# Kernel optimization log

Measured on AMD Instinct MI355X. Metric: run time of the kernel, lower is better.

Reference implementation:

```python
import jax, jax.numpy as jnp
import numpy as np

B, H, NI, NO, T = 128, 256, 2, 10, 64
LAMBDA, ETA, SAMPLE, DECISION = 0.95, 0.5, 32, 8


def _xavier(key, shape):
    fan_in, fan_out = shape
    s = (2.0 / (fan_in + fan_out)) ** 0.5
    return jax.random.normal(key, shape, dtype=jnp.float32) * s


def setup_inputs():
    key = jax.random.key(0)
    ks = jax.random.split(key, 10)
    return {
        "x_in": jax.random.normal(ks[0], (T, B, 5), dtype=jnp.float32),
        "W_sr": _xavier(ks[1], (NI, H)),
        "W_ma": _xavier(ks[2], (NI + 1, H)),
        "W_ro": _xavier(ks[3], (H, H)),
        "W_ao": _xavier(ks[4], (H, H)),
        "W_ar": _xavier(ks[5], (H, H)),
        "W_ra": _xavier(ks[6], (H, H)),
        "W_a": _xavier(ks[7], (H, H)),
        "W_y": _xavier(ks[8], (H, NO)),
        "g": jnp.ones((1, H), dtype=jnp.float32),
        "b": jnp.zeros((1, H), dtype=jnp.float32),
        "time": T,
    }


def _forward(x_in, W_sr, W_ma, W_ro, W_ao, W_ar, W_ra, W_a, W_y, g, b):
    Tn = x_in.shape[0]

    def step(carry, inp):
        r, a, A = carry
        x, t = inp  # x: [B,5]
        a_prev = a
        # ATN / RSC recurrent populations
        a = jax.nn.relu(x[:, NI:] @ W_ma + a @ W_a + r @ W_ra)      # [B,H]
        r = jax.nn.relu(x[:, :NI] @ W_sr + a_prev @ W_ar)           # [B,H]
        # readout through fast-weight memory A: o = ro(r) + r @ A + ao(a)
        o = r @ W_ro + jnp.einsum('bh,bhk->bk', r, A) + a @ W_ao    # [B,H]
        mu = jnp.mean(o, axis=0, keepdims=True)                     # mean over batch
        o = jax.nn.relu(g * (o - mu) + b)
        # Hebbian fast-weight update: A = lambda*A + eta * outer(o, r)
        eta_t = jnp.where(t > SAMPLE, 0.0, ETA)
        A = LAMBDA * A + eta_t * o[:, :, None] * r[:, None, :]      # [B,H,H]
        y = o @ W_y                                                 # [B,NO]
        return (r, a, A), y

    carry0 = (
        jnp.zeros((B, H), jnp.float32),
        jnp.zeros((B, H), jnp.float32),
        jnp.zeros((B, H, H), jnp.float32),
    )
    _, ys = jax.lax.scan(step, carry0, (x_in, jnp.arange(Tn)))
    return ys[-DECISION:]  # [decision, B, n_output]


def reference(x_in, W_sr, W_ma, W_ro, W_ao, W_ar, W_ra, W_a, W_y, g, b, time):
    return _forward(x_in, W_sr, W_ma, W_ro, W_ao, W_ar, W_ra, W_a, W_y, g, b)
```

## Files before the change

### kernel.cpp

```cpp
#include <hip/hip_runtime.h>
#include <hip/hip_fp16.h>


typedef unsigned long long u64;

#define HH 256
#define NSTEPS 64

#define OFF_ST 0u
#define OFF_C  262144u
#define OFF_MU 329728u
#define OFF_H  395264u
#define WS_FLOATS 460800u

#define SENT_STATE   0xBF800000BF800000ull
#define SENT_C       0xBF800000u
#define SENT_MU      0x7FC00000u
#define SENT_MU_PAIR 0x7FC000007FC00000ull

#define AGENT __HIP_MEMORY_SCOPE_AGENT
#define RLX   __ATOMIC_RELAXED

__device__ __forceinline__ u64 ld64(const u64* p){ return __hip_atomic_load(p,RLX,AGENT); }
__device__ __forceinline__ void st64s(u64* p,u64 v){ __hip_atomic_store(p,v,RLX,AGENT); }
__device__ __forceinline__ float ld32f(const float* p){ return __hip_atomic_load(p,RLX,AGENT); }
__device__ __forceinline__ void st32f(float* p,float v){ __hip_atomic_store(p,v,RLX,AGENT); }
__device__ __forceinline__ u64 pack2(float lo,float hi){
  return (u64)__float_as_uint(lo) | ((u64)__float_as_uint(hi)<<32);
}

__global__ __launch_bounds__(256) void smn_init(float* __restrict__ ws,
                                                float* __restrict__ out,
                                                const float* __restrict__ W_ro,
                                                const float* __restrict__ W_ao){
  unsigned i = blockIdx.x*256u + threadIdx.x, st = gridDim.x*256u;
  u64* stp=(u64*)(ws+OFF_ST); float* cp=ws+OFF_C; u64* mp=(u64*)(ws+OFF_MU);
  for (unsigned k=i;k<131072u;k+=st) st64s(&stp[k],SENT_STATE);
  for (unsigned k=i;k<67584u;k+=st)  st32f(&cp[k],__uint_as_float(SENT_C));
  for (unsigned k=i;k<32768u;k+=st)  st64s(&mp[k],SENT_MU_PAIR);
  for (unsigned k=i;k<10240u;k+=st)  out[k]=0.f;
  __half* hro = (__half*)(ws + OFF_H);
  __half* hao = hro + 65536;
  for (unsigned idx=i; idx<65536u; idx+=st) {
    unsigned k = idx >> 8, c = idx & 255u;
    unsigned dst = (c>>6)*16384u + k*64u + (c&63u);
    hro[dst] = __float2half(W_ro[idx]);
    hao[dst] = __float2half(W_ao[idx]);
  }
}

__global__ __launch_bounds__(512) void smn_main(
    const float* __restrict__ x_in, const float* __restrict__ W_sr,
    const float* __restrict__ W_ma, const float* __restrict__ W_ro,
    const float* __restrict__ W_ao, const float* __restrict__ W_ar,
    const float* __restrict__ W_ra, const float* __restrict__ W_a,
    const float* __restrict__ W_y,  const float* __restrict__ gvec,
    const float* __restrict__ bvec, float* __restrict__ out,
    float* __restrict__ ws)
{
  __shared__ __align__(16) float aF[2][HH], rF[2][HH];
  __shared__ __align__(16) float P[2][32][2][64];
  __shared__ __align__(16) float r_hist[33][2][64];
  __shared__ __align__(16) float o_hist[33][2][64];
  __shared__ __align__(8)  __half Wro_l[256][68];
  __shared__ __align__(8)  __half Wao_l[256][68];
  __shared__ float opre[2][64];
  __shared__ float c_l[33][2];
  __shared__ float mu_l[64];
  __shared__ float muG[16][32][2];
  __shared__ float lam_pow[64];
  __shared__ float x_l[2][5];

  const int tid = threadIdx.x;
  const int bid = blockIdx.x;
  const int grp = bid >> 2, jsl = bid & 3;
  const int b0 = grp * 2, c0 = jsl * 64;
  const int q = tid & 15, ks = tid >> 4;

  u64*   st64    = (u64*)(ws + OFF_ST);
  float* c_parts = ws + OFF_C;
  u64*   mu64    = (u64*)(ws + OFF_MU);

  const int cc2 = c0 + (tid & 63);
  const float gv  = gvec[cc2], bv = bvec[cc2];
  const float wma0=W_ma[cc2], wma1=W_ma[HH+cc2], wma2=W_ma[2*HH+cc2];
  const float wsr0=W_sr[cc2], wsr1=W_sr[HH+cc2];
  if (tid < 64) lam_pow[tid] = powf(0.95f,(float)tid);
  if (tid < 10) x_l[tid/5][tid%5] = x_in[(b0 + tid/5)*5 + tid%5];
  {
    const __half* hro = (const __half*)(ws + OFF_H) + jsl*16384;
    const __half* hao = (const __half*)(ws + OFF_H) + 65536 + jsl*16384;
    for (int i = tid; i < 4096; i += 512) {
      int k = i >> 4, c4 = (i & 15) * 4;
      *(uint2*)&Wro_l[k][c4] = *(const uint2*)&hro[k*64 + c4];
      *(uint2*)&Wao_l[k][c4] = *(const uint2*)&hao[k*64 + c4];
    }
  }
  __syncthreads();

  for (int t = 0; t <= NSTEPS; ++t) {
    if (t < NSTEPS) {
      if (t == 0) {
        if (tid < 128) {
          int b = tid>>6, c = tid&63;
          float va = fmaxf(x_l[b][2]*wma0 + x_l[b][3]*wma1 + x_l[b][4]*wma2, 0.f);
          float vr = fmaxf(x_l[b][0]*wsr0 + x_l[b][1]*wsr1, 0.f);
          aF[b][c0+c]=va; rF[b][c0+c]=vr; r_hist[0][b][c]=vr;
          st64s(&st64[(unsigned)((b0+b)*HH + cc2)], pack2(va,vr));
        }
        __syncthreads();
      } else {
        const int kb = ks*8;
        float sa0[8],sa1[8],sr0[8],sr1[8];
        *(float4*)&sa0[0]=*(const float4*)&aF[0][kb]; *(float4*)&sa0[4]=*(const float4*)&aF[0][kb+4];
        *(float4*)&sa1[0]=*(const float4*)&aF[1][kb]; *(float4*)&sa1[4]=*(const float4*)&aF[1][kb+4];
        *(float4*)&sr0[0]=*(const float4*)&rF[0][kb]; *(float4*)&sr0[4]=*(const float4*)&rF[0][kb+4];
        *(float4*)&sr1[0]=*(const float4*)&rF[1][kb]; *(float4*)&sr1[4]=*(const float4*)&rF[1][kb+4];
        float aA[2][4]={{0.f,0.f,0.f,0.f},{0.f,0.f,0.f,0.f}};
        float aR[2][4]={{0.f,0.f,0.f,0.f},{0.f,0.f,0.f,0.f}};
        #pragma unroll
        for (int kk=0; kk<8; ++kk) {
          const int k = kb + kk;
          const float4 wa = *(const float4*)&W_a [k*HH + c0 + q*4];
          const float4 wr = *(const float4*)&W_ra[k*HH + c0 + q*4];
          const float4 wn = *(const float4*)&W_ar[k*HH + c0 + q*4];
          #pragma unroll
          for (int jj=0;jj<4;++jj){
            const float waj=(&wa.x)[jj], wrj=(&wr.x)[jj], wnj=(&wn.x)[jj];
            aA[0][jj] += sa0[kk]*waj + sr0[kk]*wrj;
            aA[1][jj] += sa1[kk]*waj + sr1[kk]*wrj;
            aR[0][jj] += sa0[kk]*wnj;
            aR[1][jj] += sa1[kk]*wnj;
          }
        }
        *(float4*)&P[0][ks][0][q*4] = make_float4(aA[0][0],aA[0][1],aA[0][2],aA[0][3]);
        *(float4*)&P[0][ks][1][q*4] = make_float4(aA[1][0],aA[1][1],aA[1][2],aA[1][3]);
        *(float4*)&P[1][ks][0][q*4] = make_float4(aR[0][0],aR[0][1],aR[0][2],aR[0][3]);
        *(float4*)&P[1][ks][1][q*4] = make_float4(aR[1][0],aR[1][1],aR[1][2],aR[1][3]);
        __syncthreads();
        if (tid < 128) {
          int b=tid>>6, c=tid&63;
          float sa=0.f, sr=0.f;
          #pragma unroll
          for (int e=0;e<32;++e){ sa+=P[0][e][b][c]; sr+=P[1][e][b][c]; }
          float va = fmaxf(sa + x_l[b][2]*wma0 + x_l[b][3]*wma1 + x_l[b][4]*wma2, 0.f);
          float vr = fmaxf(sr + x_l[b][0]*wsr0 + x_l[b][1]*wsr1, 0.f);
          if (t<=32) r_hist[t][b][c]=vr;
          st64s(&st64[(unsigned)((t&3)*32768) + (unsigned)((b0+b)*HH + cc2)], pack2(va,vr));
          aF[b][c0+c]=va; rF[b][c0+c]=vr;
        }
        __syncthreads();
      }
      if (t+1 < NSTEPS && tid < 10)
        x_l[tid/5][tid%5] = x_in[((t+1)*128 + b0 + tid/5)*5 + tid%5];
    }

    const int tp = t - 1;
    const bool fin = (t >= 1) && (tp <= 32 || tp >= 56);
    if (fin) {
      const int m = (tp <= 32) ? tp : tp - 23;
      {
        const int p = tid & 31, ch = tid >> 5;
        const u64* base = &mu64[(unsigned)(((m&3)*4 + jsl)*64)*32u];
        u64 vals[4]; unsigned rm = 0;
        const u64* ptrs[4];
        #pragma unroll
        for (int gg=0; gg<4; ++gg) ptrs[gg] = &base[(unsigned)((ch*4+gg)*32 + p)];
        while (rm != 0xFu) {
          #pragma unroll
          for (int gg=0; gg<4; ++gg) if (!(rm & (1u<<gg))) {
            u64 v = ld64(ptrs[gg]);
            if ((unsigned)v != SENT_MU && (unsigned)(v>>32) != SENT_MU) { vals[gg]=v; rm |= 1u<<gg; }
          }
        }
        float s0=0.f, s1=0.f;
        #pragma unroll
        for (int gg=0; gg<4; ++gg) { s0 += __uint_as_float((unsigned)vals[gg]);
                                     s1 += __uint_as_float((unsigned)(vals[gg]>>32)); }
        muG[ch][p][0]=s0; muG[ch][p][1]=s1;
      }
      __syncthreads();
      if (tid < 32) {
        float s0=0.f,s1=0.f;
        #pragma unroll
        for (int ch2=0;ch2<16;++ch2){ s0+=muG[ch2][tid][0]; s1+=muG[ch2][tid][1]; }
        mu_l[2*tid]=s0*(1.f/128.f); mu_l[2*tid+1]=s1*(1.f/128.f);
        st64s(&mu64[(unsigned)((((m+3)&3)*4 + jsl)*64 + grp)*32u + (unsigned)tid], SENT_MU_PAIR);
      }
      __syncthreads();
      if (tid < 128) {
        int b=tid>>6, c=tid&63;
        float o = fmaxf(gv*(opre[b][c]-mu_l[c]) + bv, 0.f);
        opre[b][c]=o;
        if (tp<=32) o_hist[tp][b][c]=o;
      }
      __syncthreads();
      if (tp >= 56 && tid < 320) {
        int ow=tid>>4, l16=tid&15, b=ow/10, n=ow%10;
        float acc=0.f;
        #pragma unroll
        for (int i2=0;i2<4;++i2){ int c=l16*4+i2; acc += opre[b][c]*W_y[(c0+c)*10+n]; }
        acc+=__shfl_xor(acc,1); acc+=__shfl_xor(acc,2);
        acc+=__shfl_xor(acc,4); acc+=__shfl_xor(acc,8);
        if (l16==0) atomicAdd(&out[(tp-56)*1280 + (b0+b)*10 + n], acc);
      }
    }
    if (t == NSTEPS) break;

    const bool live = (t <= 32 || t >= 56);
    const int mc = (t <= 32) ? t : t - 23;
    const int smax = (t-1 < 32) ? (t-1) : 32;

    if (tid < 128) {
      if (live && smax >= 0) {
        const int l8 = tid & 7;
        for (int pp = tid>>3; pp < (smax+1)*2; pp += 16) {
          const int s = pp>>1, b2 = pp&1;
          float acc=0.f;
          #pragma unroll
          for (int i2=0;i2<8;++i2){ int c=l8*8+i2; acc += rF[b2][c0+c]*o_hist[s][b2][c]; }
          acc+=__shfl_xor(acc,1); acc+=__shfl_xor(acc,2); acc+=__shfl_xor(acc,4);
          if (l8==0) st32f(&c_parts[(unsigned)((((mc&3)*33+s)*128 + b0+b2)*4 + jsl)], acc);
        }
      }
    } else {
      const int w = tid - 128;
      const int pi = w >> 7, w2 = w & 127, b = w2>>6, c64 = w2&63;
      const int jp = (jsl + 1 + pi) & 3;
      const u64* ptr = &st64[(unsigned)((t&3)*32768) + (unsigned)((b0+b)*HH + jp*64 + c64)];
      u64 v;
      for (;;){ v = ld64(ptr); if (v != SENT_STATE) break; }
      aF[b][jp*64+c64] = __uint_as_float((unsigned)v);
      rF[b][jp*64+c64] = __uint_as_float((unsigned)(v>>32));
    }
    __syncthreads();
    if (tid < 128) {
      int b=tid>>6;
      st64s(&st64[(unsigned)(((t+3)&3)*32768) + (unsigned)((b0+b)*HH + cc2)], SENT_STATE);
    }

    if (live) {
      const int kb = ks*8;
      float sa0[8],sa1[8],sr0[8],sr1[8];
      *(float4*)&sa0[0]=*(const float4*)&aF[0][kb]; *(float4*)&sa0[4]=*(const float4*)&aF[0][kb+4];
      *(float4*)&sa1[0]=*(const float4*)&aF[1][kb]; *(float4*)&sa1[4]=*(const float4*)&aF[1][kb+4];
      *(float4*)&sr0[0]=*(const float4*)&rF[0][kb]; *(float4*)&sr0[4]=*(const float4*)&rF[0][kb+4];
      *(float4*)&sr1[0]=*(const float4*)&rF[1][kb]; *(float4*)&sr1[4]=*(const float4*)&rF[1][kb+4];
      float aO[2][4]={{0.f,0.f,0.f,0.f},{0.f,0.f,0.f,0.f}};
      #pragma unroll
      for (int kk=0;kk<8;++kk){
        const int k=kb+kk;
        const __half2* ro2 = (const __half2*)&Wro_l[k][q*4];
        const __half2* ao2 = (const __half2*)&Wao_l[k][q*4];
        const float2 wo01 = __half22float2(ro2[0]), wo23 = __half22float2(ro2[1]);
        const float2 wq01 = __half22float2(ao2[0]), wq23 = __half22float2(ao2[1]);
        const float wof[4] = {wo01.x, wo01.y, wo23.x, wo23.y};
        const float wqf[4] = {wq01.x, wq01.y, wq23.x, wq23.y};
        #pragma unroll
        for (int jj=0;jj<4;++jj){
          aO[0][jj] += sr0[kk]*wof[jj] + sa0[kk]*wqf[jj];
          aO[1][jj] += sr1[kk]*wof[jj] + sa1[kk]*wqf[jj];
        }
      }
      *(float4*)&P[0][ks][0][q*4] = make_float4(aO[0][0],aO[0][1],aO[0][2],aO[0][3]);
      *(float4*)&P[0][ks][1][q*4] = make_float4(aO[1][0],aO[1][1],aO[1][2],aO[1][3]);
      if (smax >= 0 && tid < (smax+1)*8) {
        const int s=tid>>3, b2=(tid>>2)&1, jj2=tid&3;
        const float* ptr=&c_parts[(unsigned)((((mc&3)*33+s)*128 + b0+b2)*4 + jj2)];
        float v;
        for(;;){ v=ld32f(ptr); if (__float_as_uint(v)!=SENT_C) break; }
        v+=__shfl_xor(v,1); v+=__shfl_xor(v,2);
        if (jj2==0) c_l[s][b2]=v;
      }
      __syncthreads();
      if (smax >= 0 && tid >= 128 && tid < 194) {
        const int s=(tid-128)>>1, b2=(tid-128)&1;
        st32f(&c_parts[(unsigned)(((((mc+3)&3)*33+s)*128 + b0+b2)*4 + jsl)],
              __uint_as_float(SENT_C));
      }
      if (tid < 128) {
        int b=tid>>6, c=tid&63;
        float s=0.f;
        #pragma unroll
        for (int e=0;e<32;++e) s+=P[0][e][b][c];
        for (int s2=0;s2<=smax;++s2)
          s += lam_pow[t-1-s2]*0.5f*c_l[s2][b]*r_hist[s2][b][c];
        opre[b][c]=s;
      }
      __syncthreads();
      if (tid < 32) {
        float plo=opre[0][2*tid]+opre[1][2*tid];
        float phi=opre[0][2*tid+1]+opre[1][2*tid+1];
        st64s(&mu64[(unsigned)(((mc&3)*4 + jsl)*64 + grp)*32u + (unsigned)tid], pack2(plo,phi));
      }
    }
  }
}

extern "C" void kernel_launch(void* const* d_in, const int* in_sizes, int n_in,
                              void* d_out, int out_size, void* d_ws, size_t ws_size,
                              hipStream_t stream) {
  if (ws_size < (size_t)WS_FLOATS * 4) return;
  const float* x_in = (const float*)d_in[0];
  const float* W_sr = (const float*)d_in[1];
  const float* W_ma = (const float*)d_in[2];
  const float* W_ro = (const float*)d_in[3];
  const float* W_ao = (const float*)d_in[4];
  const float* W_ar = (const float*)d_in[5];
  const float* W_ra = (const float*)d_in[6];
  const float* W_a  = (const float*)d_in[7];
  const float* W_y  = (const float*)d_in[8];
  const float* g    = (const float*)d_in[9];
  const float* b    = (const float*)d_in[10];
  float* out = (float*)d_out;
  float* ws  = (float*)d_ws;

  hipLaunchKernelGGL(smn_init, dim3(256), dim3(256), 0, stream, ws, out, W_ro, W_ao);
  hipLaunchKernelGGL(smn_main, dim3(256), dim3(512), 0, stream,
                     x_in, W_sr, W_ma, W_ro, W_ao, W_ar, W_ra, W_a, W_y, g, b,
                     out, ws);
}
```

Measured before the change: 379.9 us.

## Replace cross-block partial dot-product exchange with full o-history broadcast

Each block used to compute partial r·o dot products over its own 64-column slice and exchange them through sentinel-polled global slots. Now each block publishes its o slice to a write-once global history, pulls the other three slices, keeps the full 256-wide o history in shared memory and computes the complete dot products locally. This removes one extra global handshake and sentinel reset per step, at the cost of more global traffic and a larger workspace. The same change also drops the fp16 shared-memory copies of W_ro/W_ao, so the readout matmul now reads fp32 weights straight from global memory each step. That gives back exact precision but adds per-step global loads.

Result: slower. 401.8 us (+5.8%).

```diff
diff --git a/kernel.cpp b/kernel.cpp
--- a/kernel.cpp
+++ b/kernel.cpp
@@ -1,5 +1,4 @@
 #include <hip/hip_runtime.h>
-#include <hip/hip_fp16.h>
 
 
 typedef unsigned long long u64;
@@ -8,13 +7,11 @@
 #define NSTEPS 64
 
 #define OFF_ST 0u
-#define OFF_C  262144u
-#define OFF_MU 329728u
-#define OFF_H  395264u
-#define WS_FLOATS 460800u
+#define OFF_O  262144u
+#define OFF_MU 1343488u
+#define WS_FLOATS 1409024u
 
 #define SENT_STATE   0xBF800000BF800000ull
-#define SENT_C       0xBF800000u
 #define SENT_MU      0x7FC00000u
 #define SENT_MU_PAIR 0x7FC000007FC00000ull
 
@@ -23,30 +20,18 @@
 
 __device__ __forceinline__ u64 ld64(const u64* p){ return __hip_atomic_load(p,RLX,AGENT); }
 __device__ __forceinline__ void st64s(u64* p,u64 v){ __hip_atomic_store(p,v,RLX,AGENT); }
-__device__ __forceinline__ float ld32f(const float* p){ return __hip_atomic_load(p,RLX,AGENT); }
-__device__ __forceinline__ void st32f(float* p,float v){ __hip_atomic_store(p,v,RLX,AGENT); }
 __device__ __forceinline__ u64 pack2(float lo,float hi){
   return (u64)__float_as_uint(lo) | ((u64)__float_as_uint(hi)<<32);
 }
 
 __global__ __launch_bounds__(256) void smn_init(float* __restrict__ ws,
-                                                float* __restrict__ out,
-                                                const float* __restrict__ W_ro,
-                                                const float* __restrict__ W_ao){
+                                                float* __restrict__ out){
   unsigned i = blockIdx.x*256u + threadIdx.x, st = gridDim.x*256u;
-  u64* stp=(u64*)(ws+OFF_ST); float* cp=ws+OFF_C; u64* mp=(u64*)(ws+OFF_MU);
+  u64* stp=(u64*)(ws+OFF_ST); u64* op=(u64*)(ws+OFF_O); u64* mp=(u64*)(ws+OFF_MU);
   for (unsigned k=i;k<131072u;k+=st) st64s(&stp[k],SENT_STATE);
-  for (unsigned k=i;k<67584u;k+=st)  st32f(&cp[k],__uint_as_float(SENT_C));
+  for (unsigned k=i;k<540672u;k+=st) st64s(&op[k],SENT_STATE);
   for (unsigned k=i;k<32768u;k+=st)  st64s(&mp[k],SENT_MU_PAIR);
   for (unsigned k=i;k<10240u;k+=st)  out[k]=0.f;
-  __half* hro = (__half*)(ws + OFF_H);
-  __half* hao = hro + 65536;
-  for (unsigned idx=i; idx<65536u; idx+=st) {
-    unsigned k = idx >> 8, c = idx & 255u;
-    unsigned dst = (c>>6)*16384u + k*64u + (c&63u);
-    hro[dst] = __float2half(W_ro[idx]);
-    hao[dst] = __float2half(W_ao[idx]);
-  }
 }
 
 __global__ __launch_bounds__(512) void smn_main(
@@ -61,9 +46,7 @@
   __shared__ __align__(16) float aF[2][HH], rF[2][HH];
   __shared__ __align__(16) float P[2][32][2][64];
   __shared__ __align__(16) float r_hist[33][2][64];
-  __shared__ __align__(16) float o_hist[33][2][64];
-  __shared__ __align__(8)  __half Wro_l[256][68];
-  __shared__ __align__(8)  __half Wao_l[256][68];
+  __shared__ __align__(16) float o_hist[33][2][HH];
   __shared__ float opre[2][64];
   __shared__ float c_l[33][2];
   __shared__ float mu_l[64];
@@ -77,9 +60,9 @@
   const int b0 = grp * 2, c0 = jsl * 64;
   const int q = tid & 15, ks = tid >> 4;
 
-  u64*   st64    = (u64*)(ws + OFF_ST);
-  float* c_parts = ws + OFF_C;
-  u64*   mu64    = (u64*)(ws + OFF_MU);
+  u64* st64 = (u64*)(ws + OFF_ST);
+  u64* o64  = (u64*)(ws + OFF_O);
+  u64* mu64 = (u64*)(ws + OFF_MU);
 
   const int cc2 = c0 + (tid & 63);
   const float gv  = gvec[cc2], bv = bvec[cc2];
@@ -87,15 +70,6 @@
   const float wsr0=W_sr[cc2], wsr1=W_sr[HH+cc2];
   if (tid < 64) lam_pow[tid] = powf(0.95f,(float)tid);
   if (tid < 10) x_l[tid/5][tid%5] = x_in[(b0 + tid/5)*5 + tid%5];
-  {
-    const __half* hro = (const __half*)(ws + OFF_H) + jsl*16384;
-    const __half* hao = (const __half*)(ws + OFF_H) + 65536 + jsl*16384;
-    for (int i = tid; i < 4096; i += 512) {
-      int k = i >> 4, c4 = (i & 15) * 4;
-      *(uint2*)&Wro_l[k][c4] = *(const uint2*)&hro[k*64 + c4];
-      *(uint2*)&Wao_l[k][c4] = *(const uint2*)&hao[k*64 + c4];
-    }
-  }
   __syncthreads();
 
   for (int t = 0; t <= NSTEPS; ++t) {
@@ -192,9 +166,13 @@
         int b=tid>>6, c=tid&63;
         float o = fmaxf(gv*(opre[b][c]-mu_l[c]) + bv, 0.f);
         opre[b][c]=o;
-        if (tp<=32) o_hist[tp][b][c]=o;
-      }
-      __syncthreads();
+        if (tp<=32) o_hist[tp][b][c0+c]=o;
+      }
+      __syncthreads();
+      if (tp <= 32 && tid < 64) {
+        st64s(&o64[(unsigned)((tp*64 + grp)*HH) + (unsigned)(c0 + tid)],
+              pack2(opre[0][tid], opre[1][tid]));
+      }
       if (tp >= 56 && tid < 320) {
         int ow=tid>>4, l16=tid&15, b=ow/10, n=ow%10;
         float acc=0.f;
@@ -211,19 +189,7 @@
     const int mc = (t <= 32) ? t : t - 23;
     const int smax = (t-1 < 32) ? (t-1) : 32;
 
-    if (tid < 128) {
-      if (live && smax >= 0) {
-        const int l8 = tid & 7;
-        for (int pp = tid>>3; pp < (smax+1)*2; pp += 16) {
-          const int s = pp>>1, b2 = pp&1;
-          float acc=0.f;
-          #pragma unroll
-          for (int i2=0;i2<8;++i2){ int c=l8*8+i2; acc += rF[b2][c0+c]*o_hist[s][b2][c]; }
-          acc+=__shfl_xor(acc,1); acc+=__shfl_xor(acc,2); acc+=__shfl_xor(acc,4);
-          if (l8==0) st32f(&c_parts[(unsigned)((((mc&3)*33+s)*128 + b0+b2)*4 + jsl)], acc);
-        }
-      }
-    } else {
+    if (tid >= 128) {
       const int w = tid - 128;
       const int pi = w >> 7, w2 = w & 127, b = w2>>6, c64 = w2&63;
       const int jp = (jsl + 1 + pi) & 3;
@@ -232,6 +198,27 @@
       for (;;){ v = ld64(ptr); if (v != SENT_STATE) break; }
       aF[b][jp*64+c64] = __uint_as_float((unsigned)v);
       rF[b][jp*64+c64] = __uint_as_float((unsigned)(v>>32));
+    } else if (tid < 96 && t >= 1 && tp <= 32) {
+      const u64* ptrs[2]; int cols[2]; u64 vals[2]; unsigned rm = 0;
+      #pragma unroll
+      for (int i=0;i<2;++i) {
+        int idx = tid*2 + i;
+        int jp = (jsl + 1 + (idx>>6)) & 3, c64 = idx & 63;
+        cols[i] = jp*64 + c64;
+        ptrs[i] = &o64[(unsigned)((tp*64 + grp)*HH) + (unsigned)cols[i]];
+      }
+      while (rm != 3u) {
+        #pragma unroll
+        for (int i=0;i<2;++i) if (!(rm & (1u<<i))) {
+          u64 v = ld64(ptrs[i]);
+          if (v != SENT_STATE) { vals[i]=v; rm |= 1u<<i; }
+        }
+      }
+      #pragma unroll
+      for (int i=0;i<2;++i) {
+        o_hist[tp][0][cols[i]] = __uint_as_float((unsigned)vals[i]);
+        o_hist[tp][1][cols[i]] = __uint_as_float((unsigned)(vals[i]>>32));
+      }
     }
     __syncthreads();
     if (tid < 128) {
@@ -240,6 +227,23 @@
     }
 
     if (live) {
+      const int l8 = tid & 7;
+      for (int pp = tid>>3; pp < (smax+1)*2; pp += 64) {
+        const int s = pp>>1, b2 = pp&1;
+        float acc = 0.f;
+        #pragma unroll
+        for (int j=0;j<4;++j) {
+          const int cb = j*64 + l8*8;
+          #pragma unroll
+          for (int i2=0;i2<4;++i2) {
+            const float2 rv = *(const float2*)&rF[b2][cb + i2*2];
+            const float2 ov = *(const float2*)&o_hist[s][b2][cb + i2*2];
+            acc += rv.x*ov.x + rv.y*ov.y;
+          }
+        }
+        acc+=__shfl_xor(acc,1); acc+=__shfl_xor(acc,2); acc+=__shfl_xor(acc,4);
+        if (l8==0) c_l[s][b2]=acc;
+      }
       const int kb = ks*8;
       float sa0[8],sa1[8],sr0[8],sr1[8];
       *(float4*)&sa0[0]=*(const float4*)&aF[0][kb]; *(float4*)&sa0[4]=*(const float4*)&aF[0][kb+4];
@@ -250,34 +254,17 @@
       #pragma unroll
       for (int kk=0;kk<8;++kk){
         const int k=kb+kk;
-        const __half2* ro2 = (const __half2*)&Wro_l[k][q*4];
-        const __half2* ao2 = (const __half2*)&Wao_l[k][q*4];
-        const float2 wo01 = __half22float2(ro2[0]), wo23 = __half22float2(ro2[1]);
-        const float2 wq01 = __half22float2(ao2[0]), wq23 = __half22float2(ao2[1]);
-        const float wof[4] = {wo01.x, wo01.y, wo23.x, wo23.y};
-        const float wqf[4] = {wq01.x, wq01.y, wq23.x, wq23.y};
+        const float4 wo=*(const float4*)&W_ro[k*HH + c0 + q*4];
+        const float4 wq=*(const float4*)&W_ao[k*HH + c0 + q*4];
         #pragma unroll
         for (int jj=0;jj<4;++jj){
-          aO[0][jj] += sr0[kk]*wof[jj] + sa0[kk]*wqf[jj];
-          aO[1][jj] += sr1[kk]*wof[jj] + sa1[kk]*wqf[jj];
+          aO[0][jj] += sr0[kk]*(&wo.x)[jj] + sa0[kk]*(&wq.x)[jj];
+          aO[1][jj] += sr1[kk]*(&wo.x)[jj] + sa1[kk]*(&wq.x)[jj];
         }
       }
       *(float4*)&P[0][ks][0][q*4] = make_float4(aO[0][0],aO[0][1],aO[0][2],aO[0][3]);
       *(float4*)&P[0][ks][1][q*4] = make_float4(aO[1][0],aO[1][1],aO[1][2],aO[1][3]);
-      if (smax >= 0 && tid < (smax+1)*8) {
-        const int s=tid>>3, b2=(tid>>2)&1, jj2=tid&3;
-        const float* ptr=&c_parts[(unsigned)((((mc&3)*33+s)*128 + b0+b2)*4 + jj2)];
-        float v;
-        for(;;){ v=ld32f(ptr); if (__float_as_uint(v)!=SENT_C) break; }
-        v+=__shfl_xor(v,1); v+=__shfl_xor(v,2);
-        if (jj2==0) c_l[s][b2]=v;
-      }
-      __syncthreads();
-      if (smax >= 0 && tid >= 128 && tid < 194) {
-        const int s=(tid-128)>>1, b2=(tid-128)&1;
-        st32f(&c_parts[(unsigned)(((((mc+3)&3)*33+s)*128 + b0+b2)*4 + jsl)],
-              __uint_as_float(SENT_C));
-      }
+      __syncthreads();
       if (tid < 128) {
         int b=tid>>6, c=tid&63;
         float s=0.f;
@@ -315,7 +302,7 @@
   float* out = (float*)d_out;
   float* ws  = (float*)d_ws;
 
-  hipLaunchKernelGGL(smn_init, dim3(256), dim3(256), 0, stream, ws, out, W_ro, W_ao);
+  hipLaunchKernelGGL(smn_init, dim3(256), dim3(256), 0, stream, ws, out);
   hipLaunchKernelGGL(smn_main, dim3(256), dim3(512), 0, stream,
                      x_in, W_sr, W_ma, W_ro, W_ao, W_ar, W_ra, W_a, W_y, g, b,
                      out, ws);
```

## Detect same-XCC block groups and use L2-scoped polling for intra-group exchange

Applied to the files above, without the earlier changes.

Each block records its XCC id, and each 4-block group checks whether all members landed on the same XCC. If they did, the inter-block state, c_parts and sentinel exchanges use sc0 loads and stores (L2-coherent within one XCC) instead of agent-scope atomics, which aims to cut cross-die coherence latency on the polling path. The fp16 LDS copies of W_ro/W_ao and their conversion in the init kernel are removed; the readout now reads fp32 weights straight from global memory. A padding LDS array is added, apparently to limit occupancy so block placement is more predictable. It adds a startup handshake and relies on the XCC_ID hardware register and the sc0 semantics being correct.

Measured after the change: 384.1 us. About the same (+1.1%).

```diff
diff --git a/kernel.cpp b/kernel.cpp
--- a/kernel.cpp
+++ b/kernel.cpp
@@ -1,5 +1,4 @@
 #include <hip/hip_runtime.h>
-#include <hip/hip_fp16.h>
 
 
 typedef unsigned long long u64;
@@ -7,11 +6,11 @@
 #define HH 256
 #define NSTEPS 64
 
-#define OFF_ST 0u
-#define OFF_C  262144u
-#define OFF_MU 329728u
-#define OFF_H  395264u
-#define WS_FLOATS 460800u
+#define OFF_ST  0u
+#define OFF_C   262144u
+#define OFF_MU  329728u
+#define OFF_XCC 395264u
+#define WS_FLOATS 395520u
 
 #define SENT_STATE   0xBF800000BF800000ull
 #define SENT_C       0xBF800000u
@@ -25,28 +24,34 @@
 __device__ __forceinline__ void st64s(u64* p,u64 v){ __hip_atomic_store(p,v,RLX,AGENT); }
 __device__ __forceinline__ float ld32f(const float* p){ return __hip_atomic_load(p,RLX,AGENT); }
 __device__ __forceinline__ void st32f(float* p,float v){ __hip_atomic_store(p,v,RLX,AGENT); }
+__device__ __forceinline__ u64 ld64_l2(const u64* p){
+  u64 v; asm volatile("global_load_dwordx2 %0, %1, off sc0\ns_waitcnt vmcnt(0)"
+                      :"=v"(v):"v"(p):"memory"); return v;
+}
+__device__ __forceinline__ void st64_l2(u64* p,u64 v){
+  asm volatile("global_store_dwordx2 %0, %1, off sc0"::"v"(p),"v"(v):"memory");
+}
+__device__ __forceinline__ float ld32_l2(const float* p){
+  float v; asm volatile("global_load_dword %0, %1, off sc0\ns_waitcnt vmcnt(0)"
+                        :"=v"(v):"v"(p):"memory"); return v;
+}
+__device__ __forceinline__ void st32_l2(float* p,float v){
+  asm volatile("global_store_dword %0, %1, off sc0"::"v"(p),"v"(v):"memory");
+}
 __device__ __forceinline__ u64 pack2(float lo,float hi){
   return (u64)__float_as_uint(lo) | ((u64)__float_as_uint(hi)<<32);
 }
 
 __global__ __launch_bounds__(256) void smn_init(float* __restrict__ ws,
-                                                float* __restrict__ out,
-                                                const float* __restrict__ W_ro,
-                                                const float* __restrict__ W_ao){
+                                                float* __restrict__ out){
   unsigned i = blockIdx.x*256u + threadIdx.x, st = gridDim.x*256u;
   u64* stp=(u64*)(ws+OFF_ST); float* cp=ws+OFF_C; u64* mp=(u64*)(ws+OFF_MU);
+  int* xp=(int*)(ws+OFF_XCC);
   for (unsigned k=i;k<131072u;k+=st) st64s(&stp[k],SENT_STATE);
   for (unsigned k=i;k<67584u;k+=st)  st32f(&cp[k],__uint_as_float(SENT_C));
   for (unsigned k=i;k<32768u;k+=st)  st64s(&mp[k],SENT_MU_PAIR);
+  for (unsigned k=i;k<256u;k+=st)    __hip_atomic_store(&xp[k], -1, RLX, AGENT);
   for (unsigned k=i;k<10240u;k+=st)  out[k]=0.f;
-  __half* hro = (__half*)(ws + OFF_H);
-  __half* hao = hro + 65536;
-  for (unsigned idx=i; idx<65536u; idx+=st) {
-    unsigned k = idx >> 8, c = idx & 255u;
-    unsigned dst = (c>>6)*16384u + k*64u + (c&63u);
-    hro[dst] = __float2half(W_ro[idx]);
-    hao[dst] = __float2half(W_ao[idx]);
-  }
 }
 
 __global__ __launch_bounds__(512) void smn_main(
@@ -62,14 +67,14 @@
   __shared__ __align__(16) float P[2][32][2][64];
   __shared__ __align__(16) float r_hist[33][2][64];
   __shared__ __align__(16) float o_hist[33][2][64];
-  __shared__ __align__(8)  __half Wro_l[256][68];
-  __shared__ __align__(8)  __half Wao_l[256][68];
   __shared__ float opre[2][64];
   __shared__ float c_l[33][2];
   __shared__ float mu_l[64];
   __shared__ float muG[16][32][2];
   __shared__ float lam_pow[64];
   __shared__ float x_l[2][5];
+  __shared__ int   fastF;
+  __shared__ float lds_pad[8192];
 
   const int tid = threadIdx.x;
   const int bid = blockIdx.x;
@@ -80,6 +85,23 @@
   u64*   st64    = (u64*)(ws + OFF_ST);
   float* c_parts = ws + OFF_C;
   u64*   mu64    = (u64*)(ws + OFF_MU);
+  int*   xcc_arr = (int*)(ws + OFF_XCC);
+
+  if (out == nullptr) lds_pad[tid] = 1.f;
+
+  {
+    unsigned myxcc;
+    asm volatile("s_getreg_b32 %0, hwreg(HW_REG_XCC_ID)" : "=s"(myxcc));
+    if (tid == 0) {
+      __hip_atomic_store(&xcc_arr[bid], (int)myxcc, RLX, AGENT);
+      int e[4];
+      #pragma unroll
+      for (int i=0;i<4;++i) {
+        do { e[i] = __hip_atomic_load(&xcc_arr[grp*4+i], RLX, AGENT); } while (e[i] < 0);
+      }
+      fastF = (e[0]==e[1] && e[1]==e[2] && e[2]==e[3]) ? 1 : 0;
+    }
+  }
 
   const int cc2 = c0 + (tid & 63);
   const float gv  = gvec[cc2], bv = bvec[cc2];
@@ -87,16 +109,8 @@
   const float wsr0=W_sr[cc2], wsr1=W_sr[HH+cc2];
   if (tid < 64) lam_pow[tid] = powf(0.95f,(float)tid);
   if (tid < 10) x_l[tid/5][tid%5] = x_in[(b0 + tid/5)*5 + tid%5];
-  {
-    const __half* hro = (const __half*)(ws + OFF_H) + jsl*16384;
-    const __half* hao = (const __half*)(ws + OFF_H) + 65536 + jsl*16384;
-    for (int i = tid; i < 4096; i += 512) {
-      int k = i >> 4, c4 = (i & 15) * 4;
-      *(uint2*)&Wro_l[k][c4] = *(const uint2*)&hro[k*64 + c4];
-      *(uint2*)&Wao_l[k][c4] = *(const uint2*)&hao[k*64 + c4];
-    }
-  }
   __syncthreads();
+  const bool fast = (fastF != 0);
 
   for (int t = 0; t <= NSTEPS; ++t) {
     if (t < NSTEPS) {
@@ -106,7 +120,8 @@
           float va = fmaxf(x_l[b][2]*wma0 + x_l[b][3]*wma1 + x_l[b][4]*wma2, 0.f);
           float vr = fmaxf(x_l[b][0]*wsr0 + x_l[b][1]*wsr1, 0.f);
           aF[b][c0+c]=va; rF[b][c0+c]=vr; r_hist[0][b][c]=vr;
-          st64s(&st64[(unsigned)((b0+b)*HH + cc2)], pack2(va,vr));
+          u64* p = &st64[(unsigned)((b0+b)*HH + cc2)];
+          if (fast) st64_l2(p, pack2(va,vr)); else st64s(p, pack2(va,vr));
         }
         __syncthreads();
       } else {
@@ -146,7 +161,8 @@
           float va = fmaxf(sa + x_l[b][2]*wma0 + x_l[b][3]*wma1 + x_l[b][4]*wma2, 0.f);
           float vr = fmaxf(sr + x_l[b][0]*wsr0 + x_l[b][1]*wsr1, 0.f);
           if (t<=32) r_hist[t][b][c]=vr;
-          st64s(&st64[(unsigned)((t&3)*32768) + (unsigned)((b0+b)*HH + cc2)], pack2(va,vr));
+          u64* p = &st64[(unsigned)((t&3)*32768) + (unsigned)((b0+b)*HH + cc2)];
+          if (fast) st64_l2(p, pack2(va,vr)); else st64s(p, pack2(va,vr));
           aF[b][c0+c]=va; rF[b][c0+c]=vr;
         }
         __syncthreads();
@@ -220,7 +236,10 @@
           #pragma unroll
           for (int i2=0;i2<8;++i2){ int c=l8*8+i2; acc += rF[b2][c0+c]*o_hist[s][b2][c]; }
           acc+=__shfl_xor(acc,1); acc+=__shfl_xor(acc,2); acc+=__shfl_xor(acc,4);
-          if (l8==0) st32f(&c_parts[(unsigned)((((mc&3)*33+s)*128 + b0+b2)*4 + jsl)], acc);
+          if (l8==0) {
+            float* p = &c_parts[(unsigned)((((mc&3)*33+s)*128 + b0+b2)*4 + jsl)];
+            if (fast) st32_l2(p, acc); else st32f(p, acc);
+          }
         }
       }
     } else {
@@ -229,14 +248,16 @@
       const int jp = (jsl + 1 + pi) & 3;
       const u64* ptr = &st64[(unsigned)((t&3)*32768) + (unsigned)((b0+b)*HH + jp*64 + c64)];
       u64 v;
-      for (;;){ v = ld64(ptr); if (v != SENT_STATE) break; }
+      if (fast) { for (;;){ v = ld64_l2(ptr); if (v != SENT_STATE) break; } }
+      else      { for (;;){ v = ld64(ptr);    if (v != SENT_STATE) break; } }
       aF[b][jp*64+c64] = __uint_as_float((unsigned)v);
       rF[b][jp*64+c64] = __uint_as_float((unsigned)(v>>32));
     }
     __syncthreads();
     if (tid < 128) {
       int b=tid>>6;
-      st64s(&st64[(unsigned)(((t+3)&3)*32768) + (unsigned)((b0+b)*HH + cc2)], SENT_STATE);
+      u64* p = &st64[(unsigned)(((t+3)&3)*32768) + (unsigned)((b0+b)*HH + cc2)];
+      if (fast) st64_l2(p, SENT_STATE); else st64s(p, SENT_STATE);
     }
 
     if (live) {
@@ -250,16 +271,12 @@
       #pragma unroll
       for (int kk=0;kk<8;++kk){
         const int k=kb+kk;
-        const __half2* ro2 = (const __half2*)&Wro_l[k][q*4];
-        const __half2* ao2 = (const __half2*)&Wao_l[k][q*4];
-        const float2 wo01 = __half22float2(ro2[0]), wo23 = __half22float2(ro2[1]);
-        const float2 wq01 = __half22float2(ao2[0]), wq23 = __half22float2(ao2[1]);
-        const float wof[4] = {wo01.x, wo01.y, wo23.x, wo23.y};
-        const float wqf[4] = {wq01.x, wq01.y, wq23.x, wq23.y};
+        const float4 wo=*(const float4*)&W_ro[k*HH + c0 + q*4];
+        const float4 wq=*(const float4*)&W_ao[k*HH + c0 + q*4];
         #pragma unroll
         for (int jj=0;jj<4;++jj){
-          aO[0][jj] += sr0[kk]*wof[jj] + sa0[kk]*wqf[jj];
-          aO[1][jj] += sr1[kk]*wof[jj] + sa1[kk]*wqf[jj];
+          aO[0][jj] += sr0[kk]*(&wo.x)[jj] + sa0[kk]*(&wq.x)[jj];
+          aO[1][jj] += sr1[kk]*(&wo.x)[jj] + sa1[kk]*(&wq.x)[jj];
         }
       }
       *(float4*)&P[0][ks][0][q*4] = make_float4(aO[0][0],aO[0][1],aO[0][2],aO[0][3]);
@@ -268,15 +285,16 @@
         const int s=tid>>3, b2=(tid>>2)&1, jj2=tid&3;
         const float* ptr=&c_parts[(unsigned)((((mc&3)*33+s)*128 + b0+b2)*4 + jj2)];
         float v;
-        for(;;){ v=ld32f(ptr); if (__float_as_uint(v)!=SENT_C) break; }
+        if (fast) { for(;;){ v=ld32_l2(ptr); if (__float_as_uint(v)!=SENT_C) break; } }
+        else      { for(;;){ v=ld32f(ptr);   if (__float_as_uint(v)!=SENT_C) break; } }
         v+=__shfl_xor(v,1); v+=__shfl_xor(v,2);
         if (jj2==0) c_l[s][b2]=v;
       }
       __syncthreads();
       if (smax >= 0 && tid >= 128 && tid < 194) {
         const int s=(tid-128)>>1, b2=(tid-128)&1;
-        st32f(&c_parts[(unsigned)(((((mc+3)&3)*33+s)*128 + b0+b2)*4 + jsl)],
-              __uint_as_float(SENT_C));
+        float* p = &c_parts[(unsigned)(((((mc+3)&3)*33+s)*128 + b0+b2)*4 + jsl)];
+        if (fast) st32_l2(p, __uint_as_float(SENT_C)); else st32f(p, __uint_as_float(SENT_C));
       }
       if (tid < 128) {
         int b=tid>>6, c=tid&63;
@@ -315,7 +333,7 @@
   float* out = (float*)d_out;
   float* ws  = (float*)d_ws;
 
-  hipLaunchKernelGGL(smn_init, dim3(256), dim3(256), 0, stream, ws, out, W_ro, W_ao);
+  hipLaunchKernelGGL(smn_init, dim3(256), dim3(256), 0, stream, ws, out);
   hipLaunchKernelGGL(smn_main, dim3(256), dim3(512), 0, stream,
                      x_in, W_sr, W_ma, W_ro, W_ao, W_ar, W_ra, W_a, W_y, g, b,
                      out, ws);
```

## Drop fp16 weight staging and remove several per-step block barriers

Applied to the files above, without the earlier changes.

Removes the fp16 conversion of W_ro/W_ao in the init kernel and the shared-memory staging; the readout GEMV now reads fp32 weights directly from global memory (L2/cache). Several __syncthreads per step are eliminated by merging the batch-mean reduction into the normalization threads, producing the mu partial sums with wave shuffles, using a separate PB buffer so readout partials do not alias the recurrent P buffer, and moving the x prefetch. This cuts barrier and init overhead but adds global weight loads each step and changes numerics from fp16 to fp32 weights.

After: 394.7 us. +3.9%, slower.

```diff
diff --git a/kernel.cpp b/kernel.cpp
--- a/kernel.cpp
+++ b/kernel.cpp
@@ -1,5 +1,4 @@
 #include <hip/hip_runtime.h>
-#include <hip/hip_fp16.h>
 
 
 typedef unsigned long long u64;
@@ -10,8 +9,7 @@
 #define OFF_ST 0u
 #define OFF_C  262144u
 #define OFF_MU 329728u
-#define OFF_H  395264u
-#define WS_FLOATS 460800u
+#define WS_FLOATS 395264u
 
 #define SENT_STATE   0xBF800000BF800000ull
 #define SENT_C       0xBF800000u
@@ -30,23 +28,13 @@
 }
 
 __global__ __launch_bounds__(256) void smn_init(float* __restrict__ ws,
-                                                float* __restrict__ out,
-                                                const float* __restrict__ W_ro,
-                                                const float* __restrict__ W_ao){
+                                                float* __restrict__ out){
   unsigned i = blockIdx.x*256u + threadIdx.x, st = gridDim.x*256u;
   u64* stp=(u64*)(ws+OFF_ST); float* cp=ws+OFF_C; u64* mp=(u64*)(ws+OFF_MU);
   for (unsigned k=i;k<131072u;k+=st) st64s(&stp[k],SENT_STATE);
   for (unsigned k=i;k<67584u;k+=st)  st32f(&cp[k],__uint_as_float(SENT_C));
   for (unsigned k=i;k<32768u;k+=st)  st64s(&mp[k],SENT_MU_PAIR);
   for (unsigned k=i;k<10240u;k+=st)  out[k]=0.f;
-  __half* hro = (__half*)(ws + OFF_H);
-  __half* hao = hro + 65536;
-  for (unsigned idx=i; idx<65536u; idx+=st) {
-    unsigned k = idx >> 8, c = idx & 255u;
-    unsigned dst = (c>>6)*16384u + k*64u + (c&63u);
-    hro[dst] = __float2half(W_ro[idx]);
-    hao[dst] = __float2half(W_ao[idx]);
-  }
 }
 
 __global__ __launch_bounds__(512) void smn_main(
@@ -60,13 +48,11 @@
 {
   __shared__ __align__(16) float aF[2][HH], rF[2][HH];
   __shared__ __align__(16) float P[2][32][2][64];
+  __shared__ __align__(16) float PB[32][2][64];
   __shared__ __align__(16) float r_hist[33][2][64];
   __shared__ __align__(16) float o_hist[33][2][64];
-  __shared__ __align__(8)  __half Wro_l[256][68];
-  __shared__ __align__(8)  __half Wao_l[256][68];
   __shared__ float opre[2][64];
   __shared__ float c_l[33][2];
-  __shared__ float mu_l[64];
   __shared__ float muG[16][32][2];
   __shared__ float lam_pow[64];
   __shared__ float x_l[2][5];
@@ -87,18 +73,13 @@
   const float wsr0=W_sr[cc2], wsr1=W_sr[HH+cc2];
   if (tid < 64) lam_pow[tid] = powf(0.95f,(float)tid);
   if (tid < 10) x_l[tid/5][tid%5] = x_in[(b0 + tid/5)*5 + tid%5];
-  {
-    const __half* hro = (const __half*)(ws + OFF_H) + jsl*16384;
-    const __half* hao = (const __half*)(ws + OFF_H) + 65536 + jsl*16384;
-    for (int i = tid; i < 4096; i += 512) {
-      int k = i >> 4, c4 = (i & 15) * 4;
-      *(uint2*)&Wro_l[k][c4] = *(const uint2*)&hro[k*64 + c4];
-      *(uint2*)&Wao_l[k][c4] = *(const uint2*)&hao[k*64 + c4];
-    }
-  }
   __syncthreads();
 
   for (int t = 0; t <= NSTEPS; ++t) {
+    const int tp = t - 1;
+    const bool finran = (t >= 1) && (tp <= 32 || tp >= 56);
+    const bool live = (t <= 32 || t >= 56);
+
     if (t < NSTEPS) {
       if (t == 0) {
         if (tid < 128) {
@@ -108,7 +89,6 @@
           aF[b][c0+c]=va; rF[b][c0+c]=vr; r_hist[0][b][c]=vr;
           st64s(&st64[(unsigned)((b0+b)*HH + cc2)], pack2(va,vr));
         }
-        __syncthreads();
       } else {
         const int kb = ks*8;
         float sa0[8],sa1[8],sr0[8],sr1[8];
@@ -149,15 +129,10 @@
           st64s(&st64[(unsigned)((t&3)*32768) + (unsigned)((b0+b)*HH + cc2)], pack2(va,vr));
           aF[b][c0+c]=va; rF[b][c0+c]=vr;
         }
-        __syncthreads();
-      }
-      if (t+1 < NSTEPS && tid < 10)
-        x_l[tid/5][tid%5] = x_in[((t+1)*128 + b0 + tid/5)*5 + tid%5];
-    }
-
-    const int tp = t - 1;
-    const bool fin = (t >= 1) && (tp <= 32 || tp >= 56);
-    if (fin) {
+      }
+    }
+
+    if (finran) {
       const int m = (tp <= 32) ? tp : tp - 23;
       {
         const int p = tid & 31, ch = tid >> 5;
@@ -180,19 +155,17 @@
         muG[ch][p][0]=s0; muG[ch][p][1]=s1;
       }
       __syncthreads();
-      if (tid < 32) {
-        float s0=0.f,s1=0.f;
-        #pragma unroll
-        for (int ch2=0;ch2<16;++ch2){ s0+=muG[ch2][tid][0]; s1+=muG[ch2][tid][1]; }
-        mu_l[2*tid]=s0*(1.f/128.f); mu_l[2*tid+1]=s1*(1.f/128.f);
-        st64s(&mu64[(unsigned)((((m+3)&3)*4 + jsl)*64 + grp)*32u + (unsigned)tid], SENT_MU_PAIR);
-      }
-      __syncthreads();
       if (tid < 128) {
         int b=tid>>6, c=tid&63;
-        float o = fmaxf(gv*(opre[b][c]-mu_l[c]) + bv, 0.f);
+        float mv = 0.f;
+        #pragma unroll
+        for (int ch2=0; ch2<16; ++ch2) mv += muG[ch2][c>>1][c&1];
+        float o = fmaxf(gv*(opre[b][c] - mv*(1.0f/128.0f)) + bv, 0.f);
         opre[b][c]=o;
         if (tp<=32) o_hist[tp][b][c]=o;
+      } else if (tid < 160) {
+        st64s(&mu64[(unsigned)((((m+3)&3)*4 + jsl)*64 + grp)*32u + (unsigned)(tid-128)],
+              SENT_MU_PAIR);
       }
       __syncthreads();
       if (tp >= 56 && tid < 320) {
@@ -207,9 +180,10 @@
     }
     if (t == NSTEPS) break;
 
-    const bool live = (t <= 32 || t >= 56);
     const int mc = (t <= 32) ? t : t - 23;
     const int smax = (t-1 < 32) ? (t-1) : 32;
+
+    if (live && !finran && t > 0) __syncthreads();
 
     if (tid < 128) {
       if (live && smax >= 0) {
@@ -238,6 +212,8 @@
       int b=tid>>6;
       st64s(&st64[(unsigned)(((t+3)&3)*32768) + (unsigned)((b0+b)*HH + cc2)], SENT_STATE);
     }
+    if (t+1 < NSTEPS && tid < 10)
+      x_l[tid/5][tid%5] = x_in[((t+1)*128 + b0 + tid/5)*5 + tid%5];
 
     if (live) {
       const int kb = ks*8;
@@ -250,20 +226,16 @@
       #pragma unroll
       for (int kk=0;kk<8;++kk){
         const int k=kb+kk;
-        const __half2* ro2 = (const __half2*)&Wro_l[k][q*4];
-        const __half2* ao2 = (const __half2*)&Wao_l[k][q*4];
-        const float2 wo01 = __half22float2(ro2[0]), wo23 = __half22float2(ro2[1]);
-        const float2 wq01 = __half22float2(ao2[0]), wq23 = __half22float2(ao2[1]);
-        const float wof[4] = {wo01.x, wo01.y, wo23.x, wo23.y};
-        const float wqf[4] = {wq01.x, wq01.y, wq23.x, wq23.y};
+        const float4 wo=*(const float4*)&W_ro[k*HH + c0 + q*4];
+        const float4 wq=*(const float4*)&W_ao[k*HH + c0 + q*4];
         #pragma unroll
         for (int jj=0;jj<4;++jj){
-          aO[0][jj] += sr0[kk]*wof[jj] + sa0[kk]*wqf[jj];
-          aO[1][jj] += sr1[kk]*wof[jj] + sa1[kk]*wqf[jj];
-        }
-      }
-      *(float4*)&P[0][ks][0][q*4] = make_float4(aO[0][0],aO[0][1],aO[0][2],aO[0][3]);
-      *(float4*)&P[0][ks][1][q*4] = make_float4(aO[1][0],aO[1][1],aO[1][2],aO[1][3]);
+          aO[0][jj] += sr0[kk]*(&wo.x)[jj] + sa0[kk]*(&wq.x)[jj];
+          aO[1][jj] += sr1[kk]*(&wo.x)[jj] + sa1[kk]*(&wq.x)[jj];
+        }
+      }
+      *(float4*)&PB[ks][0][q*4] = make_float4(aO[0][0],aO[0][1],aO[0][2],aO[0][3]);
+      *(float4*)&PB[ks][1][q*4] = make_float4(aO[1][0],aO[1][1],aO[1][2],aO[1][3]);
       if (smax >= 0 && tid < (smax+1)*8) {
         const int s=tid>>3, b2=(tid>>2)&1, jj2=tid&3;
         const float* ptr=&c_parts[(unsigned)((((mc&3)*33+s)*128 + b0+b2)*4 + jj2)];
@@ -279,19 +251,19 @@
               __uint_as_float(SENT_C));
       }
       if (tid < 128) {
-        int b=tid>>6, c=tid&63;
+        int b = tid & 1, c = tid >> 1;
         float s=0.f;
         #pragma unroll
-        for (int e=0;e<32;++e) s+=P[0][e][b][c];
+        for (int e=0;e<32;++e) s+=PB[e][b][c];
         for (int s2=0;s2<=smax;++s2)
           s += lam_pow[t-1-s2]*0.5f*c_l[s2][b]*r_hist[s2][b][c];
         opre[b][c]=s;
-      }
-      __syncthreads();
-      if (tid < 32) {
-        float plo=opre[0][2*tid]+opre[1][2*tid];
-        float phi=opre[0][2*tid+1]+opre[1][2*tid+1];
-        st64s(&mu64[(unsigned)(((mc&3)*4 + jsl)*64 + grp)*32u + (unsigned)tid], pack2(plo,phi));
+        float v2 = s + __shfl_xor(s, 1);
+        float hi = __shfl_xor(v2, 2);
+        if ((tid & 3) == 0) {
+          st64s(&mu64[(unsigned)(((mc&3)*4 + jsl)*64 + grp)*32u + (unsigned)(tid>>2)],
+                pack2(v2, hi));
+        }
       }
     }
   }
@@ -315,7 +287,7 @@
   float* out = (float*)d_out;
   float* ws  = (float*)d_ws;
 
-  hipLaunchKernelGGL(smn_init, dim3(256), dim3(256), 0, stream, ws, out, W_ro, W_ao);
+  hipLaunchKernelGGL(smn_init, dim3(256), dim3(256), 0, stream, ws, out);
   hipLaunchKernelGGL(smn_main, dim3(256), dim3(512), 0, stream,
                      x_in, W_sr, W_ma, W_ro, W_ao, W_ar, W_ra, W_a, W_y, g, b,
                      out, ws);
```
